# Kernel tuning notes

Hardware: AMD Instinct MI355X
Metric: run time of the kernel (lower is better)

## Reference

```python
import jax, jax.numpy as jnp
import numpy as np

BS = 8
LEVEL = 128.0 / 255.0

RGB2YCC = jnp.array([[0.299, 0.587, 0.114],
                     [-0.168735892, -0.331264108, 0.5],
                     [0.5, -0.418687589, -0.081312411]], dtype=jnp.float32)
YCC2RGB = jnp.array([[1.0, 0.0, 1.402],
                     [1.0, -0.344136286, -0.714136286],
                     [1.0, 1.772, 0.0]], dtype=jnp.float32)


def _dctmtx(bs=BS):
    i = np.arange(bs)[:, None]
    j = np.arange(bs)[None, :]
    m = np.sqrt(2.0 / bs) * np.cos(np.pi * (2 * j + 1) * i / (2 * bs))
    m[0, :] = 1.0 / np.sqrt(bs)
    return jnp.asarray(m, dtype=jnp.float32)

DCT = _dctmtx()


def _blockify(x, bs=BS):
    # [B,H,W] -> [B,H/bs,W/bs,bs,bs]
    B, H, W = x.shape
    return x.reshape(B, H // bs, bs, W // bs, bs).transpose(0, 1, 3, 2, 4)


def _deblockify(x):
    B, hb, wb, bs, _ = x.shape
    return x.transpose(0, 1, 3, 2, 4).reshape(B, hb * bs, wb * bs)


def _round_ste(x):
    return x + jax.lax.stop_gradient(jnp.round(x) - x)


def _clamp_ste(x, lo, hi):
    return x + jax.lax.stop_gradient(jnp.clip(x, lo, hi) - x)


def setup_inputs() -> dict:
    key = jax.random.key(0)
    k1, k2 = jax.random.split(key)
    inp = jax.random.uniform(k1, (32, 3, 512, 512), dtype=jnp.float32)
    quantize = jax.random.uniform(k2, (3, BS, BS), dtype=jnp.float32,
                                  minval=40.0 / 255.0, maxval=50.0 / 255.0)
    return {"input": inp, "quantize": quantize}


def reference(input, quantize):
    B, _, H, W = input.shape
    off = jnp.array([0.0, LEVEL, LEVEL], dtype=jnp.float32)[None, :, None, None]

    # RGB -> YCbCr (plain clamp), then level shift -128/255 on all channels
    ycc = jnp.einsum('bchw,kc->bkhw', input, RGB2YCC)
    ycc = jnp.clip(ycc + off, 0.0, 1.0) - LEVEL

    # chroma 4:2:0 subsample: 2x2 mean pooling
    y = ycc[:, 0]
    cb = ycc[:, 1].reshape(B, H // 2, 2, W // 2, 2).mean(axis=(2, 4))
    cr = ycc[:, 2].reshape(B, H // 2, 2, W // 2, 2).mean(axis=(2, 4))

    # Faithful: eval path uses rounded qtable; quantize[0] used for ALL channels
    qtable = jnp.round(quantize[0] * 255.0) / 255.0

    def codec(ch):
        blk = _blockify(ch)                      # [B,hb,wb,8,8]
        d = DCT @ blk @ DCT.T                    # blockwise 2D DCT
        dec = _round_ste(d / qtable) * qtable    # straight-through quantize
        idct = DCT.T @ dec @ DCT                 # blockwise 2D IDCT
        return _deblockify(idct)

    y2, cb2, cr2 = codec(y), codec(cb), codec(cr)

    up = lambda c: jnp.repeat(jnp.repeat(c, 2, axis=1), 2, axis=2)
    ycc2 = jnp.stack([y2, up(cb2), up(cr2)], axis=1) + LEVEL

    # YCbCr -> RGB: subtract 128/255 from chroma only, matmul, STE clamp
    ycc2 = ycc2 - off
    rgb = jnp.einsum('bchw,kc->bkhw', ycc2, YCC2RGB)
    return _clamp_ste(rgb, 0.0, 1.0)
```

## Files before the change

kernel.cpp:

```cpp
#include <hip/hip_runtime.h>
#include <cmath>


#define LEVELD 0.5019607843137255
#define LEVELF 0.5019607843137255f
#define BAND   5.0e-5f

#define CA  0.35355339059327373f
#define CB0 0.49039264020161522f
#define CB1 0.41573480615127262f
#define CB2 0.27778511650980114f
#define CB3 0.09754516100806413f
#define CC0 0.46193976625564337f
#define CC1 0.19134171618254489f

__device__ const double DMATD[64] = {
  0.3535533905932738,  0.3535533905932738,  0.3535533905932738,  0.3535533905932738,
  0.3535533905932738,  0.3535533905932738,  0.3535533905932738,  0.3535533905932738,
  0.4903926402016152,  0.4157348061512726,  0.2777851165098011,  0.0975451610080641,
 -0.0975451610080641, -0.2777851165098011, -0.4157348061512726, -0.4903926402016152,
  0.4619397662556434,  0.1913417161825449, -0.1913417161825449, -0.4619397662556434,
 -0.4619397662556434, -0.1913417161825449,  0.1913417161825449,  0.4619397662556434,
  0.4157348061512726, -0.0975451610080641, -0.4903926402016152, -0.2777851165098011,
  0.2777851165098011,  0.4903926402016152,  0.0975451610080641, -0.4157348061512726,
  0.3535533905932738, -0.3535533905932738, -0.3535533905932738,  0.3535533905932738,
  0.3535533905932738, -0.3535533905932738, -0.3535533905932738,  0.3535533905932738,
  0.2777851165098011, -0.4903926402016152,  0.0975451610080641,  0.4157348061512726,
 -0.4157348061512726, -0.0975451610080641,  0.4903926402016152, -0.2777851165098011,
  0.1913417161825449, -0.4619397662556434,  0.4619397662556434, -0.1913417161825449,
 -0.1913417161825449,  0.4619397662556434, -0.4619397662556434,  0.1913417161825449,
  0.0975451610080641, -0.2777851165098011,  0.4157348061512726, -0.4903926402016152,
  0.4903926402016152, -0.4157348061512726,  0.2777851165098011, -0.0975451610080641
};

__device__ __forceinline__ float dpp_xor1(float x) {
  return __int_as_float(__builtin_amdgcn_mov_dpp(__float_as_int(x), 0xB1, 0xF, 0xF, true));
}
__device__ __forceinline__ float dpp_xor2(float x) {
  return __int_as_float(__builtin_amdgcn_mov_dpp(__float_as_int(x), 0x4E, 0xF, 0xF, true));
}
__device__ __forceinline__ float dpp_xor4(float x) {
  int t = __builtin_amdgcn_mov_dpp(__float_as_int(x), 0x141, 0xF, 0xF, true);
  return __int_as_float(__builtin_amdgcn_mov_dpp(t, 0x1B, 0xF, 0xF, true));
}

__device__ __forceinline__ void transpose8(float v[8], int p) {
  { float t[8];
    #pragma unroll
    for (int j = 0; j < 8; ++j) t[j] = dpp_xor1(v[j ^ 1]);
    const bool lb = (p & 1) != 0;
    #pragma unroll
    for (int j = 0; j < 8; ++j) v[j] = (lb == ((j & 1) != 0)) ? v[j] : t[j];
  }
  { float t[8];
    #pragma unroll
    for (int j = 0; j < 8; ++j) t[j] = dpp_xor2(v[j ^ 2]);
    const bool lb = (p & 2) != 0;
    #pragma unroll
    for (int j = 0; j < 8; ++j) v[j] = (lb == ((j & 2) != 0)) ? v[j] : t[j];
  }
  { float t[8];
    #pragma unroll
    for (int j = 0; j < 8; ++j) t[j] = dpp_xor4(v[j ^ 4]);
    const bool lb = (p & 4) != 0;
    #pragma unroll
    for (int j = 0; j < 8; ++j) v[j] = (lb == ((j & 4) != 0)) ? v[j] : t[j];
  }
}

__device__ __forceinline__ void fdct8b(float x[8]) {
  const float s0 = x[0] + x[7], s1 = x[1] + x[6], s2 = x[2] + x[5], s3 = x[3] + x[4];
  const float d0 = x[0] - x[7], d1 = x[1] - x[6], d2 = x[2] - x[5], d3 = x[3] - x[4];
  const float t0 = s0 + s3, t1 = s1 + s2, t2 = s0 - s3, t3 = s1 - s2;
  x[0] = CA * (t0 + t1);
  x[4] = CA * (t0 - t1);
  x[2] = fmaf(CC0, t2,  CC1 * t3);
  x[6] = fmaf(CC1, t2, -CC0 * t3);
  x[1] = fmaf(CB0, d0, fmaf( CB1, d1, fmaf( CB2, d2,  CB3 * d3)));
  x[3] = fmaf(CB1, d0, fmaf(-CB3, d1, fmaf(-CB0, d2, -CB2 * d3)));
  x[5] = fmaf(CB2, d0, fmaf(-CB0, d1, fmaf( CB3, d2,  CB1 * d3)));
  x[7] = fmaf(CB3, d0, fmaf(-CB2, d1, fmaf( CB1, d2, -CB0 * d3)));
}
__device__ __forceinline__ void idct8b(float y[8]) {
  const float pe = CA * (y[0] + y[4]), qe = CA * (y[0] - y[4]);
  const float re = fmaf(CC0, y[2],  CC1 * y[6]);
  const float se = fmaf(CC1, y[2], -CC0 * y[6]);
  const float E0 = pe + re, E3 = pe - re, E1 = qe + se, E2 = qe - se;
  const float O0 = fmaf(CB0, y[1], fmaf( CB1, y[3], fmaf( CB2, y[5],  CB3 * y[7])));
  const float O1 = fmaf(CB1, y[1], fmaf(-CB3, y[3], fmaf(-CB0, y[5], -CB2 * y[7])));
  const float O2 = fmaf(CB2, y[1], fmaf(-CB0, y[3], fmaf( CB3, y[5],  CB1 * y[7])));
  const float O3 = fmaf(CB3, y[1], fmaf(-CB2, y[3], fmaf( CB1, y[5], -CB0 * y[7])));
  y[0] = E0 + O0; y[7] = E0 - O0;
  y[1] = E1 + O1; y[6] = E1 - O1;
  y[2] = E2 + O2; y[5] = E2 - O2;
  y[3] = E3 + O3; y[4] = E3 - O3;
}

__device__ __attribute__((noinline)) float rescue_coef(
    const float* __restrict__ quant, const float* __restrict__ base,
    int mode, int i, int j)
{
  double acc = 0.0;
  if (mode == 0) {
    #pragma unroll 1
    for (int k = 0; k < 8; ++k) {
      double e = 0.0;
      #pragma unroll
      for (int l = 0; l < 8; ++l) {
        const size_t off = (size_t)k * 512 + l;
        const double rr = (double)base[off];
        const double gg = (double)base[262144 + off];
        const double bb = (double)base[524288 + off];
        double y = 0.299 * rr + 0.587 * gg + 0.114 * bb;
        y = fmin(fmax(y, 0.0), 1.0) - LEVELD;
        e += y * DMATD[j * 8 + l];
      }
      acc += DMATD[i * 8 + k] * e;
    }
  } else {
    const double c0 = (mode == 1) ? -0.168735892 : 0.5;
    const double c1 = (mode == 1) ? -0.331264108 : -0.418687589;
    const double c2 = (mode == 1) ?  0.5         : -0.081312411;
    #pragma unroll 1
    for (int k = 0; k < 8; ++k) {
      double e = 0.0;
      #pragma unroll 1
      for (int l = 0; l < 8; ++l) {
        double m = 0.0;
        #pragma unroll
        for (int dr = 0; dr < 2; ++dr)
          #pragma unroll
          for (int dc = 0; dc < 2; ++dc) {
            const size_t off = (size_t)(2 * k + dr) * 512 + (2 * l + dc);
            const double rr = (double)base[off];
            const double gg = (double)base[262144 + off];
            const double bb = (double)base[524288 + off];
            const double v = c0 * rr + c1 * gg + c2 * bb;
            m += fmin(fmax(v + LEVELD, 0.0), 1.0) - LEVELD;
          }
        e += (0.25 * m) * DMATD[j * 8 + l];
      }
      acc += DMATD[i * 8 + k] * e;
    }
  }
  const double qd = rint((double)quant[i * 8 + j] * 255.0) * (1.0 / 255.0);
  return (float)(rint(acc / qd) * qd);
}

__device__ __forceinline__ void codec8(float x[8], const float qv[8], const float rq[8],
                                       int p, int mode, const float* __restrict__ base,
                                       const float* __restrict__ quant)
{
  fdct8b(x); transpose8(x, p); fdct8b(x);
  unsigned bad = 0u;
  #pragma unroll
  for (int i = 0; i < 8; ++i) {
    const float tt = x[i] * rq[i];
    const float rt = rintf(tt);
    if (fabsf(tt - rt) > 0.5f - BAND) bad |= (1u << i);
    x[i] = rt * qv[i];
  }
  if (__builtin_expect(bad != 0u, 0)) {
    do {
      const int i = __builtin_ctz(bad);
      bad &= bad - 1u;
      const float fix = rescue_coef(quant, base, mode, i, p);
      #pragma unroll
      for (int k = 0; k < 8; ++k) x[k] = (k == i) ? fix : x[k];
    } while (bad != 0u);
  }
  idct8b(x); transpose8(x, p); idct8b(x);
}

__device__ __forceinline__ void color_stage(
    const float4 L6[6], int tY, int qr, int qc, int p,
    float4* __restrict__ CHW, float rout[8])
{
  const float RL[8] = {L6[0].x, L6[0].y, L6[0].z, L6[0].w, L6[1].x, L6[1].y, L6[1].z, L6[1].w};
  const float GL[8] = {L6[2].x, L6[2].y, L6[2].z, L6[2].w, L6[3].x, L6[3].y, L6[3].z, L6[3].w};
  const float BL[8] = {L6[4].x, L6[4].y, L6[4].z, L6[4].w, L6[5].x, L6[5].y, L6[5].z, L6[5].w};

  float cbv[8], crv[8];
  #pragma unroll
  for (int l = 0; l < 8; ++l) {
    const float rr = RL[l], gg = GL[l], bb = BL[l];
    const float y  = fmaf(0.114f, bb, fmaf(0.587f, gg, 0.299f * rr));
    const float cb = fmaf(0.5f, bb, fmaf(-0.331264108f, gg, -0.168735892f * rr));
    const float cr = fmaf(-0.081312411f, bb, fmaf(-0.418687589f, gg, 0.5f * rr));
    rout[l] = fminf(fmaxf(y,           0.0f), 1.0f) - LEVELF;
    cbv[l]  = fminf(fmaxf(cb + LEVELF, 0.0f), 1.0f) - LEVELF;
    crv[l]  = fminf(fmaxf(cr + LEVELF, 0.0f), 1.0f) - LEVELF;
  }
  float ch[4];
  #pragma unroll
  for (int j = 0; j < 4; ++j) {
    const float cbh = cbv[2 * j] + cbv[2 * j + 1];
    const float crh = crv[2 * j] + crv[2 * j + 1];
    const float cbs = cbh + dpp_xor1(cbh);
    const float crs = crh + dpp_xor1(crh);
    ch[j] = 0.25f * ((p & 1) ? crs : cbs);
  }
  const int crow = qr * 4 + (p >> 1);
  const int slot = ((((p & 1) * 4 + tY) * 16) + crow * 2 + qc) ^ ((tY << 1) | qr);
  CHW[slot] = make_float4(ch[0], ch[1], ch[2], ch[3]);
}

__device__ __forceinline__ void out_phase(
    float* __restrict__ ob, int tY, int qr, int qc, int p,
    const float4* __restrict__ CHW, const float r[8])
{
  const int crow = qr * 4 + (p >> 1);
  const int swz = (tY << 1) | qr;
  const float4 cb4 = CHW[((tY * 16) + crow * 2 + qc) ^ swz];
  const float4 cr4 = CHW[(((4 + tY) * 16) + crow * 2 + qc) ^ swz];
  const float cba[4] = {cb4.x, cb4.y, cb4.z, cb4.w};
  const float cra[4] = {cr4.x, cr4.y, cr4.z, cr4.w};

  float RR[8], GG[8], BB[8];
  #pragma unroll
  for (int l = 0; l < 8; ++l) {
    const float y2 = r[l] + LEVELF;
    const float cbb = cba[l >> 1], crr = cra[l >> 1];
    float ro = fmaf(1.402f, crr, y2);
    float go = y2 - 0.344136286f * cbb - 0.714136286f * crr;
    float bo = fmaf(1.772f, cbb, y2);
    RR[l] = fminf(fmaxf(ro, 0.0f), 1.0f);
    GG[l] = fminf(fmaxf(go, 0.0f), 1.0f);
    BB[l] = fminf(fmaxf(bo, 0.0f), 1.0f);
  }
  float* op = ob + (size_t)(qr * 8 + p) * 512 + tY * 16 + qc * 8;
  *(float4*)(op)              = make_float4(RR[0], RR[1], RR[2], RR[3]);
  *(float4*)(op + 4)          = make_float4(RR[4], RR[5], RR[6], RR[7]);
  *(float4*)(op + 262144)     = make_float4(GG[0], GG[1], GG[2], GG[3]);
  *(float4*)(op + 262148)     = make_float4(GG[4], GG[5], GG[6], GG[7]);
  *(float4*)(op + 524288)     = make_float4(BB[0], BB[1], BB[2], BB[3]);
  *(float4*)(op + 524292)     = make_float4(BB[4], BB[5], BB[6], BB[7]);
}

__global__ __launch_bounds__(64, 4) void jpeg_fused(
    const float* __restrict__ in, const float* __restrict__ quant,
    float* __restrict__ out)
{
  __shared__ float4 CH[128];

  const int lane = threadIdx.x;
  const int g = lane >> 3, p = lane & 7;
  const int tx = g >> 2, qr = (g >> 1) & 1, qc = g & 1;

  const int u    = blockIdx.x;
  const int img  = u >> 8;
  const int trow = (u >> 3) & 31;
  const int tcq  = u & 7;
  const size_t tboff = (size_t)img * 786432 + (size_t)trow * 16 * 512 + (size_t)tcq * 64;
  const float* tb = in + tboff;
  float* ob = out + tboff;

  float4 L[2][6];
  #pragma unroll
  for (int h = 0; h < 2; ++h) {
    const int tY = 2 * h + tx;
    const float* pb = tb + (size_t)(qr * 8 + p) * 512 + tY * 16 + qc * 8;
    L[h][0] = *(const float4*)(pb);
    L[h][1] = *(const float4*)(pb + 4);
    L[h][2] = *(const float4*)(pb + 262144);
    L[h][3] = *(const float4*)(pb + 262148);
    L[h][4] = *(const float4*)(pb + 524288);
    L[h][5] = *(const float4*)(pb + 524292);
  }
  float qf[8];
  #pragma unroll
  for (int i = 0; i < 8; ++i) qf[i] = quant[i * 8 + p];

  float qv[8], rq[8];
  #pragma unroll
  for (int i = 0; i < 8; ++i) {
    const double qd = rint((double)qf[i] * 255.0) * (1.0 / 255.0);
    qv[i] = (float)qd;
    rq[i] = 1.0f / qv[i];
  }

  float rA[8], rB[8];
  color_stage(L[0], 2 * 0 + tx, qr, qc, p, CH, rA);
  color_stage(L[1], 2 * 1 + tx, qr, qc, p, CH, rB);
  __builtin_amdgcn_wave_barrier();

  const float* blkA = tb + (size_t)(qr * 8) * 512 + (2 * 0 + tx) * 16 + qc * 8;
  const float* blkB = tb + (size_t)(qr * 8) * 512 + (2 * 1 + tx) * 16 + qc * 8;
  codec8(rA, qv, rq, p, 0, blkA, quant);
  codec8(rB, qv, rq, p, 0, blkB, quant);

  {
    const int cpar = g >> 2, ct = g & 3;
    const int pre  = (cpar * 4 + ct) * 16 + p * 2;
    const int swz  = (ct << 1) | (p >> 2);
    const int sl = pre ^ swz, sh = (pre + 1) ^ swz;
    const float4 a = CH[sl];
    const float4 b = CH[sh];
    float xc[8] = {a.x, a.y, a.z, a.w, b.x, b.y, b.z, b.w};
    codec8(xc, qv, rq, p, 1 + cpar, tb + ct * 16, quant);
    CH[sl] = make_float4(xc[0], xc[1], xc[2], xc[3]);
    CH[sh] = make_float4(xc[4], xc[5], xc[6], xc[7]);
  }
  __builtin_amdgcn_wave_barrier();

  out_phase(ob, 2 * 0 + tx, qr, qc, p, CH, rA);
  out_phase(ob, 2 * 1 + tx, qr, qc, p, CH, rB);
}

extern "C" void kernel_launch(void* const* d_in, const int* in_sizes, int n_in,
                              void* d_out, int out_size, void* d_ws, size_t ws_size,
                              hipStream_t stream) {
  const float* in    = (const float*)d_in[0];
  const float* quant = (const float*)d_in[1];
  float* out = (float*)d_out;

  jpeg_fused<<<dim3(8192), dim3(64), 0, stream>>>(in, quant, out);
}
```

Measured before the change: 63.77 us.

## Restructure into 256-thread band blocks staging Y and chroma in LDS

Replaces the 64-thread per-tile kernel with 256-thread blocks that each process a 16x256 band. Pixels are loaded row-contiguously, converted to YCbCr, and staged in padded LDS buffers. Blocks are then DCT-coded from LDS and the final RGB is written back in contiguous rows. The goal is wider coalesced global accesses and fewer, larger blocks. In exchange it adds block-wide __syncthreads and more LDS per block. The qtable rounding also moves from double to float precision.

```diff
diff --git a/kernel.cpp b/kernel.cpp
--- a/kernel.cpp
+++ b/kernel.cpp
@@ -172,139 +172,148 @@
   idct8b(x); transpose8(x, p); idct8b(x);
 }
 
-__device__ __forceinline__ void color_stage(
-    const float4 L6[6], int tY, int qr, int qc, int p,
-    float4* __restrict__ CHW, float rout[8])
-{
-  const float RL[8] = {L6[0].x, L6[0].y, L6[0].z, L6[0].w, L6[1].x, L6[1].y, L6[1].z, L6[1].w};
-  const float GL[8] = {L6[2].x, L6[2].y, L6[2].z, L6[2].w, L6[3].x, L6[3].y, L6[3].z, L6[3].w};
-  const float BL[8] = {L6[4].x, L6[4].y, L6[4].z, L6[4].w, L6[5].x, L6[5].y, L6[5].z, L6[5].w};
-
-  float cbv[8], crv[8];
-  #pragma unroll
-  for (int l = 0; l < 8; ++l) {
-    const float rr = RL[l], gg = GL[l], bb = BL[l];
-    const float y  = fmaf(0.114f, bb, fmaf(0.587f, gg, 0.299f * rr));
-    const float cb = fmaf(0.5f, bb, fmaf(-0.331264108f, gg, -0.168735892f * rr));
-    const float cr = fmaf(-0.081312411f, bb, fmaf(-0.418687589f, gg, 0.5f * rr));
-    rout[l] = fminf(fmaxf(y,           0.0f), 1.0f) - LEVELF;
-    cbv[l]  = fminf(fmaxf(cb + LEVELF, 0.0f), 1.0f) - LEVELF;
-    crv[l]  = fminf(fmaxf(cr + LEVELF, 0.0f), 1.0f) - LEVELF;
-  }
-  float ch[4];
-  #pragma unroll
-  for (int j = 0; j < 4; ++j) {
-    const float cbh = cbv[2 * j] + cbv[2 * j + 1];
-    const float crh = crv[2 * j] + crv[2 * j + 1];
-    const float cbs = cbh + dpp_xor1(cbh);
-    const float crs = crh + dpp_xor1(crh);
-    ch[j] = 0.25f * ((p & 1) ? crs : cbs);
-  }
-  const int crow = qr * 4 + (p >> 1);
-  const int slot = ((((p & 1) * 4 + tY) * 16) + crow * 2 + qc) ^ ((tY << 1) | qr);
-  CHW[slot] = make_float4(ch[0], ch[1], ch[2], ch[3]);
-}
-
-__device__ __forceinline__ void out_phase(
-    float* __restrict__ ob, int tY, int qr, int qc, int p,
-    const float4* __restrict__ CHW, const float r[8])
-{
-  const int crow = qr * 4 + (p >> 1);
-  const int swz = (tY << 1) | qr;
-  const float4 cb4 = CHW[((tY * 16) + crow * 2 + qc) ^ swz];
-  const float4 cr4 = CHW[(((4 + tY) * 16) + crow * 2 + qc) ^ swz];
-  const float cba[4] = {cb4.x, cb4.y, cb4.z, cb4.w};
-  const float cra[4] = {cr4.x, cr4.y, cr4.z, cr4.w};
-
-  float RR[8], GG[8], BB[8];
-  #pragma unroll
-  for (int l = 0; l < 8; ++l) {
-    const float y2 = r[l] + LEVELF;
-    const float cbb = cba[l >> 1], crr = cra[l >> 1];
-    float ro = fmaf(1.402f, crr, y2);
-    float go = y2 - 0.344136286f * cbb - 0.714136286f * crr;
-    float bo = fmaf(1.772f, cbb, y2);
-    RR[l] = fminf(fmaxf(ro, 0.0f), 1.0f);
-    GG[l] = fminf(fmaxf(go, 0.0f), 1.0f);
-    BB[l] = fminf(fmaxf(bo, 0.0f), 1.0f);
-  }
-  float* op = ob + (size_t)(qr * 8 + p) * 512 + tY * 16 + qc * 8;
-  *(float4*)(op)              = make_float4(RR[0], RR[1], RR[2], RR[3]);
-  *(float4*)(op + 4)          = make_float4(RR[4], RR[5], RR[6], RR[7]);
-  *(float4*)(op + 262144)     = make_float4(GG[0], GG[1], GG[2], GG[3]);
-  *(float4*)(op + 262148)     = make_float4(GG[4], GG[5], GG[6], GG[7]);
-  *(float4*)(op + 524288)     = make_float4(BB[0], BB[1], BB[2], BB[3]);
-  *(float4*)(op + 524292)     = make_float4(BB[4], BB[5], BB[6], BB[7]);
-}
-
-__global__ __launch_bounds__(64, 4) void jpeg_fused(
+#define YSTRIDE 260
+#define CSTRIDE 132
+
+__global__ __launch_bounds__(256, 6) void jpeg_band(
     const float* __restrict__ in, const float* __restrict__ quant,
     float* __restrict__ out)
 {
-  __shared__ float4 CH[128];
-
-  const int lane = threadIdx.x;
+  __shared__ float Ylds[16 * YSTRIDE];
+  __shared__ float Clds[2][8 * CSTRIDE];
+
+  const int t    = threadIdx.x;
+  const int wave = t >> 6;
+  const int lane = t & 63;
   const int g = lane >> 3, p = lane & 7;
-  const int tx = g >> 2, qr = (g >> 1) & 1, qc = g & 1;
-
-  const int u    = blockIdx.x;
-  const int img  = u >> 8;
-  const int trow = (u >> 3) & 31;
-  const int tcq  = u & 7;
-  const size_t tboff = (size_t)img * 786432 + (size_t)trow * 16 * 512 + (size_t)tcq * 64;
-  const float* tb = in + tboff;
-  float* ob = out + tboff;
-
-  float4 L[2][6];
-  #pragma unroll
-  for (int h = 0; h < 2; ++h) {
-    const int tY = 2 * h + tx;
-    const float* pb = tb + (size_t)(qr * 8 + p) * 512 + tY * 16 + qc * 8;
-    L[h][0] = *(const float4*)(pb);
-    L[h][1] = *(const float4*)(pb + 4);
-    L[h][2] = *(const float4*)(pb + 262144);
-    L[h][3] = *(const float4*)(pb + 262148);
-    L[h][4] = *(const float4*)(pb + 524288);
-    L[h][5] = *(const float4*)(pb + 524292);
-  }
-  float qf[8];
-  #pragma unroll
-  for (int i = 0; i < 8; ++i) qf[i] = quant[i * 8 + p];
+
+  const int band = blockIdx.x;
+  const int img  = band >> 6;
+  const int trow = (band >> 1) & 31;
+  const int half = band & 1;
+  const size_t base = (size_t)img * 786432 + (size_t)trow * 8192 + (size_t)half * 256;
 
   float qv[8], rq[8];
   #pragma unroll
   for (int i = 0; i < 8; ++i) {
-    const double qd = rint((double)qf[i] * 255.0) * (1.0 / 255.0);
-    qv[i] = (float)qd;
+    qv[i] = rintf(quant[i * 8 + p] * 255.0f) * (1.0f / 255.0f);
     rq[i] = 1.0f / qv[i];
   }
 
-  float rA[8], rB[8];
-  color_stage(L[0], 2 * 0 + tx, qr, qc, p, CH, rA);
-  color_stage(L[1], 2 * 1 + tx, qr, qc, p, CH, rB);
-  __builtin_amdgcn_wave_barrier();
-
-  const float* blkA = tb + (size_t)(qr * 8) * 512 + (2 * 0 + tx) * 16 + qc * 8;
-  const float* blkB = tb + (size_t)(qr * 8) * 512 + (2 * 1 + tx) * 16 + qc * 8;
-  codec8(rA, qv, rq, p, 0, blkA, quant);
-  codec8(rB, qv, rq, p, 0, blkB, quant);
-
   {
-    const int cpar = g >> 2, ct = g & 3;
-    const int pre  = (cpar * 4 + ct) * 16 + p * 2;
-    const int swz  = (ct << 1) | (p >> 2);
-    const int sl = pre ^ swz, sh = (pre + 1) ^ swz;
-    const float4 a = CH[sl];
-    const float4 b = CH[sh];
-    float xc[8] = {a.x, a.y, a.z, a.w, b.x, b.y, b.z, b.w};
-    codec8(xc, qv, rq, p, 1 + cpar, tb + ct * 16, quant);
-    CH[sl] = make_float4(xc[0], xc[1], xc[2], xc[3]);
-    CH[sh] = make_float4(xc[4], xc[5], xc[6], xc[7]);
-  }
-  __builtin_amdgcn_wave_barrier();
-
-  out_phase(ob, 2 * 0 + tx, qr, qc, p, CH, rA);
-  out_phase(ob, 2 * 1 + tx, qr, qc, p, CH, rB);
+    const int row = t >> 4;
+    const int c0  = (t & 15) * 16;
+    const float* pr = in + base + (size_t)row * 512 + c0;
+
+    float4 R[4], G[4], B[4];
+    #pragma unroll
+    for (int i = 0; i < 4; ++i) R[i] = *(const float4*)(pr + 4 * i);
+    #pragma unroll
+    for (int i = 0; i < 4; ++i) G[i] = *(const float4*)(pr + 262144 + 4 * i);
+    #pragma unroll
+    for (int i = 0; i < 4; ++i) B[i] = *(const float4*)(pr + 524288 + 4 * i);
+
+    float yv[16], cbv[16], crv[16];
+    #pragma unroll
+    for (int i = 0; i < 16; ++i) {
+      const float rr = ((const float*)R)[i];
+      const float gg = ((const float*)G)[i];
+      const float bb = ((const float*)B)[i];
+      const float y  = fmaf(0.114f, bb, fmaf(0.587f, gg, 0.299f * rr));
+      const float cb = fmaf(0.5f, bb, fmaf(-0.331264108f, gg, -0.168735892f * rr));
+      const float cr = fmaf(-0.081312411f, bb, fmaf(-0.418687589f, gg, 0.5f * rr));
+      yv[i]  = fminf(fmaxf(y,           0.0f), 1.0f) - LEVELF;
+      cbv[i] = fminf(fmaxf(cb + LEVELF, 0.0f), 1.0f) - LEVELF;
+      crv[i] = fminf(fmaxf(cr + LEVELF, 0.0f), 1.0f) - LEVELF;
+    }
+
+    float* yw = &Ylds[row * YSTRIDE + c0];
+    #pragma unroll
+    for (int i = 0; i < 4; ++i)
+      *(float4*)(yw + 4 * i) = make_float4(yv[4*i], yv[4*i+1], yv[4*i+2], yv[4*i+3]);
+
+    float cbh[8], crh[8];
+    #pragma unroll
+    for (int j = 0; j < 8; ++j) {
+      cbh[j] = cbv[2*j] + cbv[2*j+1];
+      crh[j] = crv[2*j] + crv[2*j+1];
+    }
+    #pragma unroll
+    for (int j = 0; j < 8; ++j) {
+      cbh[j] = 0.25f * (cbh[j] + __shfl_xor(cbh[j], 16));
+      crh[j] = 0.25f * (crh[j] + __shfl_xor(crh[j], 16));
+    }
+    if ((row & 1) == 0) {
+      float* cw0 = &Clds[0][(row >> 1) * CSTRIDE + (c0 >> 1)];
+      float* cw1 = &Clds[1][(row >> 1) * CSTRIDE + (c0 >> 1)];
+      *(float4*)(cw0)     = make_float4(cbh[0], cbh[1], cbh[2], cbh[3]);
+      *(float4*)(cw0 + 4) = make_float4(cbh[4], cbh[5], cbh[6], cbh[7]);
+      *(float4*)(cw1)     = make_float4(crh[0], crh[1], crh[2], crh[3]);
+      *(float4*)(cw1 + 4) = make_float4(crh[4], crh[5], crh[6], crh[7]);
+    }
+  }
+  __syncthreads();
+
+  #pragma unroll
+  for (int r = 0; r < 2; ++r) {
+    const int id   = r * 32 + wave * 8 + g;
+    const int brow = id >> 5, bcol = id & 31;
+    float* yr = &Ylds[(brow * 8 + p) * YSTRIDE + bcol * 8];
+    float x[8];
+    { const float4 a = *(const float4*)(yr);
+      const float4 b = *(const float4*)(yr + 4);
+      x[0]=a.x; x[1]=a.y; x[2]=a.z; x[3]=a.w; x[4]=b.x; x[5]=b.y; x[6]=b.z; x[7]=b.w; }
+    const float* gbase = in + base + (size_t)(brow * 8) * 512 + bcol * 8;
+    codec8(x, qv, rq, p, 0, gbase, quant);
+    *(float4*)(yr)     = make_float4(x[0], x[1], x[2], x[3]);
+    *(float4*)(yr + 4) = make_float4(x[4], x[5], x[6], x[7]);
+  }
+  {
+    const int cid = wave * 8 + g;
+    const int ch  = cid >> 4, bc = cid & 15;
+    float* cr_ = &Clds[ch][p * CSTRIDE + bc * 8];
+    float x[8];
+    { const float4 a = *(const float4*)(cr_);
+      const float4 b = *(const float4*)(cr_ + 4);
+      x[0]=a.x; x[1]=a.y; x[2]=a.z; x[3]=a.w; x[4]=b.x; x[5]=b.y; x[6]=b.z; x[7]=b.w; }
+    const float* gbase = in + base + bc * 16;
+    codec8(x, qv, rq, p, 1 + ch, gbase, quant);
+    *(float4*)(cr_)     = make_float4(x[0], x[1], x[2], x[3]);
+    *(float4*)(cr_ + 4) = make_float4(x[4], x[5], x[6], x[7]);
+  }
+  __syncthreads();
+
+  {
+    const int row = t >> 4;
+    const int c0  = (t & 15) * 16;
+    const float* yr = &Ylds[row * YSTRIDE + c0];
+    const float* cb8 = &Clds[0][(row >> 1) * CSTRIDE + (c0 >> 1)];
+    const float* cr8 = &Clds[1][(row >> 1) * CSTRIDE + (c0 >> 1)];
+
+    float RR[16], GG[16], BB[16];
+    #pragma unroll
+    for (int i = 0; i < 16; ++i) {
+      const float y2  = yr[i] + LEVELF;
+      const float cbb = cb8[i >> 1];
+      const float crr = cr8[i >> 1];
+      float ro = fmaf(1.402f, crr, y2);
+      float go = y2 - 0.344136286f * cbb - 0.714136286f * crr;
+      float bo = fmaf(1.772f, cbb, y2);
+      RR[i] = fminf(fmaxf(ro, 0.0f), 1.0f);
+      GG[i] = fminf(fmaxf(go, 0.0f), 1.0f);
+      BB[i] = fminf(fmaxf(bo, 0.0f), 1.0f);
+    }
+    float* po = out + base + (size_t)row * 512 + c0;
+    #pragma unroll
+    for (int i = 0; i < 4; ++i)
+      *(float4*)(po + 4 * i)          = make_float4(RR[4*i], RR[4*i+1], RR[4*i+2], RR[4*i+3]);
+    #pragma unroll
+    for (int i = 0; i < 4; ++i)
+      *(float4*)(po + 262144 + 4 * i) = make_float4(GG[4*i], GG[4*i+1], GG[4*i+2], GG[4*i+3]);
+    #pragma unroll
+    for (int i = 0; i < 4; ++i)
+      *(float4*)(po + 524288 + 4 * i) = make_float4(BB[4*i], BB[4*i+1], BB[4*i+2], BB[4*i+3]);
+  }
 }
 
 extern "C" void kernel_launch(void* const* d_in, const int* in_sizes, int n_in,
@@ -314,5 +323,5 @@
   const float* quant = (const float*)d_in[1];
   float* out = (float*)d_out;
 
-  jpeg_fused<<<dim3(8192), dim3(64), 0, stream>>>(in, quant, out);
-}
+  jpeg_band<<<dim3(2048), dim3(256), 0, stream>>>(in, quant, out);
+}
```

Result: slower. 73.07 us (+14.6%).

## Shrink work per wave to one 16x16 tile with single codec pass

Applied to the files above, without the earlier changes.

Each 64-lane block now handles one 16x16 pixel tile instead of four. Lanes 0-31 run the luma 8x8 blocks and lanes 32-47 run the Cb and Cr chroma blocks in the same codec pass. This removes the second serialized codec8 call per lane and launches four times as many blocks. In exchange, lanes 48-63 stay idle during the codec and output phases and the loads are smaller per wave. The qtable rounding also moves from double to float, which can change results at exact rounding boundaries.

```diff
diff --git a/kernel.cpp b/kernel.cpp
--- a/kernel.cpp
+++ b/kernel.cpp
@@ -147,49 +147,52 @@
   return (float)(rint(acc / qd) * qd);
 }
 
-__device__ __forceinline__ void codec8(float x[8], const float qv[8], const float rq[8],
-                                       int p, int mode, const float* __restrict__ base,
-                                       const float* __restrict__ quant)
+__global__ __launch_bounds__(64) void jpeg_fused(
+    const float* __restrict__ in, const float* __restrict__ quant,
+    float* __restrict__ out)
 {
-  fdct8b(x); transpose8(x, p); fdct8b(x);
-  unsigned bad = 0u;
+  __shared__ float CH[136];
+
+  const int lane = threadIdx.x;
+  const int g = lane >> 3, p = lane & 7;
+  const int qr = (g >> 1) & 1, qc = g & 1;
+
+  const int u    = blockIdx.x;
+  const int img  = u >> 10;
+  const int trow = (u >> 5) & 31;
+  const int tcol = u & 31;
+  const size_t tbase = (size_t)img * 786432 + (size_t)trow * 8192 + (size_t)tcol * 16;
+  const float* tb = in + tbase;
+
+  const float* pb = tb + (size_t)(qr * 8 + p) * 512 + qc * 8;
+  const float4 R0 = *(const float4*)(pb);
+  const float4 R1 = *(const float4*)(pb + 4);
+  const float4 G0 = *(const float4*)(pb + 262144);
+  const float4 G1 = *(const float4*)(pb + 262148);
+  const float4 B0 = *(const float4*)(pb + 524288);
+  const float4 B1 = *(const float4*)(pb + 524292);
+
+  float qv[8], rq[8];
   #pragma unroll
   for (int i = 0; i < 8; ++i) {
-    const float tt = x[i] * rq[i];
-    const float rt = rintf(tt);
-    if (fabsf(tt - rt) > 0.5f - BAND) bad |= (1u << i);
-    x[i] = rt * qv[i];
-  }
-  if (__builtin_expect(bad != 0u, 0)) {
-    do {
-      const int i = __builtin_ctz(bad);
-      bad &= bad - 1u;
-      const float fix = rescue_coef(quant, base, mode, i, p);
-      #pragma unroll
-      for (int k = 0; k < 8; ++k) x[k] = (k == i) ? fix : x[k];
-    } while (bad != 0u);
-  }
-  idct8b(x); transpose8(x, p); idct8b(x);
-}
-
-__device__ __forceinline__ void color_stage(
-    const float4 L6[6], int tY, int qr, int qc, int p,
-    float4* __restrict__ CHW, float rout[8])
-{
-  const float RL[8] = {L6[0].x, L6[0].y, L6[0].z, L6[0].w, L6[1].x, L6[1].y, L6[1].z, L6[1].w};
-  const float GL[8] = {L6[2].x, L6[2].y, L6[2].z, L6[2].w, L6[3].x, L6[3].y, L6[3].z, L6[3].w};
-  const float BL[8] = {L6[4].x, L6[4].y, L6[4].z, L6[4].w, L6[5].x, L6[5].y, L6[5].z, L6[5].w};
-
-  float cbv[8], crv[8];
+    qv[i] = rintf(quant[i * 8 + p] * 255.0f) * (1.0f / 255.0f);
+    rq[i] = 1.0f / qv[i];
+  }
+
+  const float RL[8] = {R0.x, R0.y, R0.z, R0.w, R1.x, R1.y, R1.z, R1.w};
+  const float GL[8] = {G0.x, G0.y, G0.z, G0.w, G1.x, G1.y, G1.z, G1.w};
+  const float BL[8] = {B0.x, B0.y, B0.z, B0.w, B1.x, B1.y, B1.z, B1.w};
+
+  float x[8], cbv[8], crv[8];
   #pragma unroll
   for (int l = 0; l < 8; ++l) {
     const float rr = RL[l], gg = GL[l], bb = BL[l];
     const float y  = fmaf(0.114f, bb, fmaf(0.587f, gg, 0.299f * rr));
     const float cb = fmaf(0.5f, bb, fmaf(-0.331264108f, gg, -0.168735892f * rr));
     const float cr = fmaf(-0.081312411f, bb, fmaf(-0.418687589f, gg, 0.5f * rr));
-    rout[l] = fminf(fmaxf(y,           0.0f), 1.0f) - LEVELF;
-    cbv[l]  = fminf(fmaxf(cb + LEVELF, 0.0f), 1.0f) - LEVELF;
-    crv[l]  = fminf(fmaxf(cr + LEVELF, 0.0f), 1.0f) - LEVELF;
+    x[l]   = fminf(fmaxf(y,           0.0f), 1.0f) - LEVELF;
+    cbv[l] = fminf(fmaxf(cb + LEVELF, 0.0f), 1.0f) - LEVELF;
+    crv[l] = fminf(fmaxf(cr + LEVELF, 0.0f), 1.0f) - LEVELF;
   }
   float ch[4];
   #pragma unroll
@@ -200,111 +203,78 @@
     const float crs = crh + dpp_xor1(crh);
     ch[j] = 0.25f * ((p & 1) ? crs : cbs);
   }
-  const int crow = qr * 4 + (p >> 1);
-  const int slot = ((((p & 1) * 4 + tY) * 16) + crow * 2 + qc) ^ ((tY << 1) | qr);
-  CHW[slot] = make_float4(ch[0], ch[1], ch[2], ch[3]);
-}
-
-__device__ __forceinline__ void out_phase(
-    float* __restrict__ ob, int tY, int qr, int qc, int p,
-    const float4* __restrict__ CHW, const float r[8])
-{
-  const int crow = qr * 4 + (p >> 1);
-  const int swz = (tY << 1) | qr;
-  const float4 cb4 = CHW[((tY * 16) + crow * 2 + qc) ^ swz];
-  const float4 cr4 = CHW[(((4 + tY) * 16) + crow * 2 + qc) ^ swz];
-  const float cba[4] = {cb4.x, cb4.y, cb4.z, cb4.w};
-  const float cra[4] = {cr4.x, cr4.y, cr4.z, cr4.w};
-
-  float RR[8], GG[8], BB[8];
-  #pragma unroll
-  for (int l = 0; l < 8; ++l) {
-    const float y2 = r[l] + LEVELF;
-    const float cbb = cba[l >> 1], crr = cra[l >> 1];
-    float ro = fmaf(1.402f, crr, y2);
-    float go = y2 - 0.344136286f * cbb - 0.714136286f * crr;
-    float bo = fmaf(1.772f, cbb, y2);
-    RR[l] = fminf(fmaxf(ro, 0.0f), 1.0f);
-    GG[l] = fminf(fmaxf(go, 0.0f), 1.0f);
-    BB[l] = fminf(fmaxf(bo, 0.0f), 1.0f);
-  }
-  float* op = ob + (size_t)(qr * 8 + p) * 512 + tY * 16 + qc * 8;
-  *(float4*)(op)              = make_float4(RR[0], RR[1], RR[2], RR[3]);
-  *(float4*)(op + 4)          = make_float4(RR[4], RR[5], RR[6], RR[7]);
-  *(float4*)(op + 262144)     = make_float4(GG[0], GG[1], GG[2], GG[3]);
-  *(float4*)(op + 262148)     = make_float4(GG[4], GG[5], GG[6], GG[7]);
-  *(float4*)(op + 524288)     = make_float4(BB[0], BB[1], BB[2], BB[3]);
-  *(float4*)(op + 524292)     = make_float4(BB[4], BB[5], BB[6], BB[7]);
-}
-
-__global__ __launch_bounds__(64, 4) void jpeg_fused(
-    const float* __restrict__ in, const float* __restrict__ quant,
-    float* __restrict__ out)
-{
-  __shared__ float4 CH[128];
-
-  const int lane = threadIdx.x;
-  const int g = lane >> 3, p = lane & 7;
-  const int tx = g >> 2, qr = (g >> 1) & 1, qc = g & 1;
-
-  const int u    = blockIdx.x;
-  const int img  = u >> 8;
-  const int trow = (u >> 3) & 31;
-  const int tcq  = u & 7;
-  const size_t tboff = (size_t)img * 786432 + (size_t)trow * 16 * 512 + (size_t)tcq * 64;
-  const float* tb = in + tboff;
-  float* ob = out + tboff;
-
-  float4 L[2][6];
-  #pragma unroll
-  for (int h = 0; h < 2; ++h) {
-    const int tY = 2 * h + tx;
-    const float* pb = tb + (size_t)(qr * 8 + p) * 512 + tY * 16 + qc * 8;
-    L[h][0] = *(const float4*)(pb);
-    L[h][1] = *(const float4*)(pb + 4);
-    L[h][2] = *(const float4*)(pb + 262144);
-    L[h][3] = *(const float4*)(pb + 262148);
-    L[h][4] = *(const float4*)(pb + 524288);
-    L[h][5] = *(const float4*)(pb + 524292);
-  }
-  float qf[8];
-  #pragma unroll
-  for (int i = 0; i < 8; ++i) qf[i] = quant[i * 8 + p];
-
-  float qv[8], rq[8];
+  if (g < 4) {
+    float* dst = &CH[(p & 1) * 68 + (qr * 4 + (p >> 1)) * 8 + qc * 4];
+    *(float4*)dst = make_float4(ch[0], ch[1], ch[2], ch[3]);
+  }
+  __builtin_amdgcn_wave_barrier();
+
+  if (g >= 4) {
+    const float* src = &CH[(g & 1) * 68 + p * 8];
+    const float4 a = *(const float4*)(src);
+    const float4 b = *(const float4*)(src + 4);
+    x[0] = a.x; x[1] = a.y; x[2] = a.z; x[3] = a.w;
+    x[4] = b.x; x[5] = b.y; x[6] = b.z; x[7] = b.w;
+  }
+  __builtin_amdgcn_wave_barrier();
+
+  fdct8b(x); transpose8(x, p); fdct8b(x);
+  unsigned bad = 0u;
   #pragma unroll
   for (int i = 0; i < 8; ++i) {
-    const double qd = rint((double)qf[i] * 255.0) * (1.0 / 255.0);
-    qv[i] = (float)qd;
-    rq[i] = 1.0f / qv[i];
-  }
-
-  float rA[8], rB[8];
-  color_stage(L[0], 2 * 0 + tx, qr, qc, p, CH, rA);
-  color_stage(L[1], 2 * 1 + tx, qr, qc, p, CH, rB);
+    const float tt = x[i] * rq[i];
+    const float rt = rintf(tt);
+    if (fabsf(tt - rt) > 0.5f - BAND) bad |= (1u << i);
+    x[i] = rt * qv[i];
+  }
+  if (g >= 6) bad = 0u;
+  if (__builtin_expect(bad != 0u, 0)) {
+    const int mode = (g < 4) ? 0 : (g == 4 ? 1 : 2);
+    const float* gbase = (g < 4) ? (tb + (size_t)(qr * 8) * 512 + qc * 8) : tb;
+    do {
+      const int i = __builtin_ctz(bad);
+      bad &= bad - 1u;
+      const float fix = rescue_coef(quant, gbase, mode, i, p);
+      #pragma unroll
+      for (int k = 0; k < 8; ++k) x[k] = (k == i) ? fix : x[k];
+    } while (bad != 0u);
+  }
+  idct8b(x); transpose8(x, p); idct8b(x);
+
+  if ((g & 6) == 4) {
+    float* dst = &CH[(g & 1) * 68 + p * 8];
+    *(float4*)(dst)     = make_float4(x[0], x[1], x[2], x[3]);
+    *(float4*)(dst + 4) = make_float4(x[4], x[5], x[6], x[7]);
+  }
   __builtin_amdgcn_wave_barrier();
 
-  const float* blkA = tb + (size_t)(qr * 8) * 512 + (2 * 0 + tx) * 16 + qc * 8;
-  const float* blkB = tb + (size_t)(qr * 8) * 512 + (2 * 1 + tx) * 16 + qc * 8;
-  codec8(rA, qv, rq, p, 0, blkA, quant);
-  codec8(rB, qv, rq, p, 0, blkB, quant);
-
-  {
-    const int cpar = g >> 2, ct = g & 3;
-    const int pre  = (cpar * 4 + ct) * 16 + p * 2;
-    const int swz  = (ct << 1) | (p >> 2);
-    const int sl = pre ^ swz, sh = (pre + 1) ^ swz;
-    const float4 a = CH[sl];
-    const float4 b = CH[sh];
-    float xc[8] = {a.x, a.y, a.z, a.w, b.x, b.y, b.z, b.w};
-    codec8(xc, qv, rq, p, 1 + cpar, tb + ct * 16, quant);
-    CH[sl] = make_float4(xc[0], xc[1], xc[2], xc[3]);
-    CH[sh] = make_float4(xc[4], xc[5], xc[6], xc[7]);
-  }
-  __builtin_amdgcn_wave_barrier();
-
-  out_phase(ob, 2 * 0 + tx, qr, qc, p, CH, rA);
-  out_phase(ob, 2 * 1 + tx, qr, qc, p, CH, rB);
+  if (g < 4) {
+    const float* cbp = &CH[(qr * 4 + (p >> 1)) * 8 + qc * 4];
+    const float4 cb4 = *(const float4*)(cbp);
+    const float4 cr4 = *(const float4*)(cbp + 68);
+    const float cba[4] = {cb4.x, cb4.y, cb4.z, cb4.w};
+    const float cra[4] = {cr4.x, cr4.y, cr4.z, cr4.w};
+
+    float RR[8], GG[8], BB[8];
+    #pragma unroll
+    for (int l = 0; l < 8; ++l) {
+      const float y2 = x[l] + LEVELF;
+      const float cbb = cba[l >> 1], crr = cra[l >> 1];
+      float ro = fmaf(1.402f, crr, y2);
+      float go = y2 - 0.344136286f * cbb - 0.714136286f * crr;
+      float bo = fmaf(1.772f, cbb, y2);
+      RR[l] = fminf(fmaxf(ro, 0.0f), 1.0f);
+      GG[l] = fminf(fmaxf(go, 0.0f), 1.0f);
+      BB[l] = fminf(fmaxf(bo, 0.0f), 1.0f);
+    }
+    float* ob = out + tbase + (size_t)(qr * 8 + p) * 512 + qc * 8;
+    *(float4*)(ob)              = make_float4(RR[0], RR[1], RR[2], RR[3]);
+    *(float4*)(ob + 4)          = make_float4(RR[4], RR[5], RR[6], RR[7]);
+    *(float4*)(ob + 262144)     = make_float4(GG[0], GG[1], GG[2], GG[3]);
+    *(float4*)(ob + 262148)     = make_float4(GG[4], GG[5], GG[6], GG[7]);
+    *(float4*)(ob + 524288)     = make_float4(BB[0], BB[1], BB[2], BB[3]);
+    *(float4*)(ob + 524292)     = make_float4(BB[4], BB[5], BB[6], BB[7]);
+  }
 }
 
 extern "C" void kernel_launch(void* const* d_in, const int* in_sizes, int n_in,
@@ -314,5 +284,5 @@
   const float* quant = (const float*)d_in[1];
   float* out = (float*)d_out;
 
-  jpeg_fused<<<dim3(8192), dim3(64), 0, stream>>>(in, quant, out);
-}
+  jpeg_fused<<<dim3(32768), dim3(64), 0, stream>>>(in, quant, out);
+}
```

New measurement: 79.71 us. 1.25x slower.

## Pack paired DCT codec blocks into float2 vectors for packed FMA

Applied to the files above, without the earlier changes.

Rewrites the 8-point DCT/IDCT and the transposes to operate on two blocks at once with float2 vectors, so the compiler can emit packed FP32 math (v_pk_fma). The two luma blocks are processed together, and the Cb/Cr chroma blocks are paired in one codec call, with half the lanes redundant and only g<4 writing back. It also computes the qtable in float instead of double. This cuts VALU instruction count but adds register pressure, duplicated chroma work on half the lanes, and a small precision change in the qtable.

```diff
diff --git a/kernel.cpp b/kernel.cpp
--- a/kernel.cpp
+++ b/kernel.cpp
@@ -13,6 +13,11 @@
 #define CB3 0.09754516100806413f
 #define CC0 0.46193976625564337f
 #define CC1 0.19134171618254489f
+
+typedef float f2 __attribute__((ext_vector_type(2)));
+
+__device__ __forceinline__ f2 pkfma(f2 a, f2 b, f2 c) { return a * b + c; }
+__device__ __forceinline__ f2 pkfma(float a, f2 b, f2 c) { f2 av = {a, a}; return av * b + c; }
 
 __device__ const double DMATD[64] = {
   0.3535533905932738,  0.3535533905932738,  0.3535533905932738,  0.3535533905932738,
@@ -43,53 +48,56 @@
   int t = __builtin_amdgcn_mov_dpp(__float_as_int(x), 0x141, 0xF, 0xF, true);
   return __int_as_float(__builtin_amdgcn_mov_dpp(t, 0x1B, 0xF, 0xF, true));
 }
-
-__device__ __forceinline__ void transpose8(float v[8], int p) {
-  { float t[8];
-    #pragma unroll
-    for (int j = 0; j < 8; ++j) t[j] = dpp_xor1(v[j ^ 1]);
+__device__ __forceinline__ f2 dpp_xor1v(f2 x) { f2 r; r.x = dpp_xor1(x.x); r.y = dpp_xor1(x.y); return r; }
+__device__ __forceinline__ f2 dpp_xor2v(f2 x) { f2 r; r.x = dpp_xor2(x.x); r.y = dpp_xor2(x.y); return r; }
+__device__ __forceinline__ f2 dpp_xor4v(f2 x) { f2 r; r.x = dpp_xor4(x.x); r.y = dpp_xor4(x.y); return r; }
+
+__device__ __forceinline__ void transpose8p(f2 v[8], int p) {
+  { f2 t[8];
+    #pragma unroll
+    for (int j = 0; j < 8; ++j) t[j] = dpp_xor1v(v[j ^ 1]);
     const bool lb = (p & 1) != 0;
     #pragma unroll
     for (int j = 0; j < 8; ++j) v[j] = (lb == ((j & 1) != 0)) ? v[j] : t[j];
   }
-  { float t[8];
-    #pragma unroll
-    for (int j = 0; j < 8; ++j) t[j] = dpp_xor2(v[j ^ 2]);
+  { f2 t[8];
+    #pragma unroll
+    for (int j = 0; j < 8; ++j) t[j] = dpp_xor2v(v[j ^ 2]);
     const bool lb = (p & 2) != 0;
     #pragma unroll
     for (int j = 0; j < 8; ++j) v[j] = (lb == ((j & 2) != 0)) ? v[j] : t[j];
   }
-  { float t[8];
-    #pragma unroll
-    for (int j = 0; j < 8; ++j) t[j] = dpp_xor4(v[j ^ 4]);
+  { f2 t[8];
+    #pragma unroll
+    for (int j = 0; j < 8; ++j) t[j] = dpp_xor4v(v[j ^ 4]);
     const bool lb = (p & 4) != 0;
     #pragma unroll
     for (int j = 0; j < 8; ++j) v[j] = (lb == ((j & 4) != 0)) ? v[j] : t[j];
   }
 }
 
-__device__ __forceinline__ void fdct8b(float x[8]) {
-  const float s0 = x[0] + x[7], s1 = x[1] + x[6], s2 = x[2] + x[5], s3 = x[3] + x[4];
-  const float d0 = x[0] - x[7], d1 = x[1] - x[6], d2 = x[2] - x[5], d3 = x[3] - x[4];
-  const float t0 = s0 + s3, t1 = s1 + s2, t2 = s0 - s3, t3 = s1 - s2;
+__device__ __forceinline__ void fdct8p(f2 x[8]) {
+  const f2 s0 = x[0] + x[7], s1 = x[1] + x[6], s2 = x[2] + x[5], s3 = x[3] + x[4];
+  const f2 d0 = x[0] - x[7], d1 = x[1] - x[6], d2 = x[2] - x[5], d3 = x[3] - x[4];
+  const f2 t0 = s0 + s3, t1 = s1 + s2, t2 = s0 - s3, t3 = s1 - s2;
   x[0] = CA * (t0 + t1);
   x[4] = CA * (t0 - t1);
-  x[2] = fmaf(CC0, t2,  CC1 * t3);
-  x[6] = fmaf(CC1, t2, -CC0 * t3);
-  x[1] = fmaf(CB0, d0, fmaf( CB1, d1, fmaf( CB2, d2,  CB3 * d3)));
-  x[3] = fmaf(CB1, d0, fmaf(-CB3, d1, fmaf(-CB0, d2, -CB2 * d3)));
-  x[5] = fmaf(CB2, d0, fmaf(-CB0, d1, fmaf( CB3, d2,  CB1 * d3)));
-  x[7] = fmaf(CB3, d0, fmaf(-CB2, d1, fmaf( CB1, d2, -CB0 * d3)));
-}
-__device__ __forceinline__ void idct8b(float y[8]) {
-  const float pe = CA * (y[0] + y[4]), qe = CA * (y[0] - y[4]);
-  const float re = fmaf(CC0, y[2],  CC1 * y[6]);
-  const float se = fmaf(CC1, y[2], -CC0 * y[6]);
-  const float E0 = pe + re, E3 = pe - re, E1 = qe + se, E2 = qe - se;
-  const float O0 = fmaf(CB0, y[1], fmaf( CB1, y[3], fmaf( CB2, y[5],  CB3 * y[7])));
-  const float O1 = fmaf(CB1, y[1], fmaf(-CB3, y[3], fmaf(-CB0, y[5], -CB2 * y[7])));
-  const float O2 = fmaf(CB2, y[1], fmaf(-CB0, y[3], fmaf( CB3, y[5],  CB1 * y[7])));
-  const float O3 = fmaf(CB3, y[1], fmaf(-CB2, y[3], fmaf( CB1, y[5], -CB0 * y[7])));
+  x[2] = pkfma(CC0, t2,  CC1 * t3);
+  x[6] = pkfma(CC1, t2, -CC0 * t3);
+  x[1] = pkfma(CB0, d0, pkfma( CB1, d1, pkfma( CB2, d2,  CB3 * d3)));
+  x[3] = pkfma(CB1, d0, pkfma(-CB3, d1, pkfma(-CB0, d2, -CB2 * d3)));
+  x[5] = pkfma(CB2, d0, pkfma(-CB0, d1, pkfma( CB3, d2,  CB1 * d3)));
+  x[7] = pkfma(CB3, d0, pkfma(-CB2, d1, pkfma( CB1, d2, -CB0 * d3)));
+}
+__device__ __forceinline__ void idct8p(f2 y[8]) {
+  const f2 pe = CA * (y[0] + y[4]), qe = CA * (y[0] - y[4]);
+  const f2 re = pkfma(CC0, y[2],  CC1 * y[6]);
+  const f2 se = pkfma(CC1, y[2], -CC0 * y[6]);
+  const f2 E0 = pe + re, E3 = pe - re, E1 = qe + se, E2 = qe - se;
+  const f2 O0 = pkfma(CB0, y[1], pkfma( CB1, y[3], pkfma( CB2, y[5],  CB3 * y[7])));
+  const f2 O1 = pkfma(CB1, y[1], pkfma(-CB3, y[3], pkfma(-CB0, y[5], -CB2 * y[7])));
+  const f2 O2 = pkfma(CB2, y[1], pkfma(-CB0, y[3], pkfma( CB3, y[5],  CB1 * y[7])));
+  const f2 O3 = pkfma(CB3, y[1], pkfma(-CB2, y[3], pkfma( CB1, y[5], -CB0 * y[7])));
   y[0] = E0 + O0; y[7] = E0 - O0;
   y[1] = E1 + O1; y[6] = E1 - O1;
   y[2] = E2 + O2; y[5] = E2 - O2;
@@ -147,29 +155,44 @@
   return (float)(rint(acc / qd) * qd);
 }
 
-__device__ __forceinline__ void codec8(float x[8], const float qv[8], const float rq[8],
-                                       int p, int mode, const float* __restrict__ base,
-                                       const float* __restrict__ quant)
-{
-  fdct8b(x); transpose8(x, p); fdct8b(x);
-  unsigned bad = 0u;
+__device__ __forceinline__ void codec8p(
+    f2 x[8], const float qv[8], const float rq[8], int p, bool doRescue,
+    const float* __restrict__ baseX, int modeX,
+    const float* __restrict__ baseY, int modeY,
+    const float* __restrict__ quant)
+{
+  fdct8p(x); transpose8p(x, p); fdct8p(x);
+  unsigned badX = 0u, badY = 0u;
   #pragma unroll
   for (int i = 0; i < 8; ++i) {
-    const float tt = x[i] * rq[i];
-    const float rt = rintf(tt);
-    if (fabsf(tt - rt) > 0.5f - BAND) bad |= (1u << i);
+    const f2 tt = x[i] * rq[i];
+    const float rtx = rintf(tt.x);
+    const float rty = rintf(tt.y);
+    if (fabsf(tt.x - rtx) > 0.5f - BAND) badX |= (1u << i);
+    if (fabsf(tt.y - rty) > 0.5f - BAND) badY |= (1u << i);
+    f2 rt = {rtx, rty};
     x[i] = rt * qv[i];
   }
-  if (__builtin_expect(bad != 0u, 0)) {
+  if (!doRescue) { badX = 0u; badY = 0u; }
+  if (__builtin_expect(badX != 0u, 0)) {
     do {
-      const int i = __builtin_ctz(bad);
-      bad &= bad - 1u;
-      const float fix = rescue_coef(quant, base, mode, i, p);
+      const int i = __builtin_ctz(badX);
+      badX &= badX - 1u;
+      const float fix = rescue_coef(quant, baseX, modeX, i, p);
       #pragma unroll
-      for (int k = 0; k < 8; ++k) x[k] = (k == i) ? fix : x[k];
-    } while (bad != 0u);
-  }
-  idct8b(x); transpose8(x, p); idct8b(x);
+      for (int k = 0; k < 8; ++k) if (k == i) x[k].x = fix;
+    } while (badX != 0u);
+  }
+  if (__builtin_expect(badY != 0u, 0)) {
+    do {
+      const int i = __builtin_ctz(badY);
+      badY &= badY - 1u;
+      const float fix = rescue_coef(quant, baseY, modeY, i, p);
+      #pragma unroll
+      for (int k = 0; k < 8; ++k) if (k == i) x[k].y = fix;
+    } while (badY != 0u);
+  }
+  idct8p(x); transpose8p(x, p); idct8p(x);
 }
 
 __device__ __forceinline__ void color_stage(
@@ -274,8 +297,7 @@
   float qv[8], rq[8];
   #pragma unroll
   for (int i = 0; i < 8; ++i) {
-    const double qd = rint((double)qf[i] * 255.0) * (1.0 / 255.0);
-    qv[i] = (float)qd;
+    qv[i] = rintf(qf[i] * 255.0f) * (1.0f / 255.0f);
     rq[i] = 1.0f / qv[i];
   }
 
@@ -284,22 +306,43 @@
   color_stage(L[1], 2 * 1 + tx, qr, qc, p, CH, rB);
   __builtin_amdgcn_wave_barrier();
 
-  const float* blkA = tb + (size_t)(qr * 8) * 512 + (2 * 0 + tx) * 16 + qc * 8;
-  const float* blkB = tb + (size_t)(qr * 8) * 512 + (2 * 1 + tx) * 16 + qc * 8;
-  codec8(rA, qv, rq, p, 0, blkA, quant);
-  codec8(rB, qv, rq, p, 0, blkB, quant);
-
   {
-    const int cpar = g >> 2, ct = g & 3;
-    const int pre  = (cpar * 4 + ct) * 16 + p * 2;
+    f2 x[8];
+    #pragma unroll
+    for (int i = 0; i < 8; ++i) { x[i].x = rA[i]; x[i].y = rB[i]; }
+    const float* blkA = tb + (size_t)(qr * 8) * 512 + (2 * 0 + tx) * 16 + qc * 8;
+    const float* blkB = tb + (size_t)(qr * 8) * 512 + (2 * 1 + tx) * 16 + qc * 8;
+    codec8p(x, qv, rq, p, true, blkA, 0, blkB, 0, quant);
+    #pragma unroll
+    for (int i = 0; i < 8; ++i) { rA[i] = x[i].x; rB[i] = x[i].y; }
+  }
+
+  {
+    const int ct = g & 3;
+    const int preB = (0 * 4 + ct) * 16 + p * 2;
+    const int preR = (1 * 4 + ct) * 16 + p * 2;
     const int swz  = (ct << 1) | (p >> 2);
-    const int sl = pre ^ swz, sh = (pre + 1) ^ swz;
-    const float4 a = CH[sl];
-    const float4 b = CH[sh];
-    float xc[8] = {a.x, a.y, a.z, a.w, b.x, b.y, b.z, b.w};
-    codec8(xc, qv, rq, p, 1 + cpar, tb + ct * 16, quant);
-    CH[sl] = make_float4(xc[0], xc[1], xc[2], xc[3]);
-    CH[sh] = make_float4(xc[4], xc[5], xc[6], xc[7]);
+    const int slB = preB ^ swz, shB = (preB + 1) ^ swz;
+    const int slR = preR ^ swz, shR = (preR + 1) ^ swz;
+    const float4 ab = CH[slB];
+    const float4 bb = CH[shB];
+    const float4 ar = CH[slR];
+    const float4 br = CH[shR];
+    f2 x[8];
+    x[0].x = ab.x; x[1].x = ab.y; x[2].x = ab.z; x[3].x = ab.w;
+    x[4].x = bb.x; x[5].x = bb.y; x[6].x = bb.z; x[7].x = bb.w;
+    x[0].y = ar.x; x[1].y = ar.y; x[2].y = ar.z; x[3].y = ar.w;
+    x[4].y = br.x; x[5].y = br.y; x[6].y = br.z; x[7].y = br.w;
+
+    codec8p(x, qv, rq, p, g < 4, tb + ct * 16, 1, tb + ct * 16, 2, quant);
+
+    __builtin_amdgcn_wave_barrier();
+    if (g < 4) {
+      CH[slB] = make_float4(x[0].x, x[1].x, x[2].x, x[3].x);
+      CH[shB] = make_float4(x[4].x, x[5].x, x[6].x, x[7].x);
+      CH[slR] = make_float4(x[0].y, x[1].y, x[2].y, x[3].y);
+      CH[shR] = make_float4(x[4].y, x[5].y, x[6].y, x[7].y);
+    }
   }
   __builtin_amdgcn_wave_barrier();
 
```

New measurement: 74.80 us. +17.3%, slower.
